# Performance work log

Hardware: AMD Instinct MI355X
Metric: run time of the kernel (lower is better)

## Reference

```python
import jax, jax.numpy as jnp
import numpy as np

B = 64        # BATCH_SIZE
C_IN = 16
L = 8192
FFT0 = 64
FFT1 = 256
CO = 32       # c_out per fft branch (c_out=64 / 2 ffts)
RATIO = FFT1 // FFT0  # 4
EPS = 1e-5


def setup_inputs() -> dict:
    key = jax.random.key(0)
    ks = jax.random.split(key, 12)
    x = jax.random.normal(ks[0], (B, C_IN, L), jnp.float32)
    bn_gamma = 1.0 + 0.1 * jax.random.normal(ks[1], (2, B), jnp.float32)
    bn_beta = 0.1 * jax.random.normal(ks[2], (2, B), jnp.float32)
    mk_r = 0.1 * jax.random.normal(ks[3], (RATIO, RATIO), jnp.float32)
    mk_i = 0.1 * jax.random.normal(ks[4], (RATIO, RATIO), jnp.float32)
    mb_r = 0.1 * jax.random.normal(ks[5], (RATIO,), jnp.float32)
    mb_i = 0.1 * jax.random.normal(ks[6], (RATIO,), jnp.float32)
    fk0_r = 0.1 * jax.random.normal(ks[7], (FFT0 // 2 + 1, C_IN, CO), jnp.float32)
    fk0_i = 0.1 * jax.random.normal(ks[8], (FFT0 // 2 + 1, C_IN, CO), jnp.float32)
    fk1_r = 0.1 * jax.random.normal(ks[9], (FFT1 // 2 + 1, C_IN, CO), jnp.float32)
    fk1_i = 0.1 * jax.random.normal(ks[10], (FFT1 // 2 + 1, C_IN, CO), jnp.float32)
    pbias = 0.1 * jax.random.normal(ks[11], (2 * CO,), jnp.float32)
    return dict(x=x, bn_gamma=bn_gamma, bn_beta=bn_beta, mk_r=mk_r, mk_i=mk_i,
                mb_r=mb_r, mb_i=mb_i, fk0_r=fk0_r, fk0_i=fk0_i,
                fk1_r=fk1_r, fk1_i=fk1_i, pbias=pbias)


def _stft(x2d, n):
    # torch.stft(center=True, pad_mode='reflect', hop=n_fft, rect window),
    # then keep onesided bins and drop the last frame (as in the module).
    N = x2d.shape[0]
    xp = jnp.pad(x2d, ((0, 0), (n // 2, n // 2)), mode='reflect')
    frames = xp.reshape(N, -1, n)               # (N, T+1, n), hop == n_fft
    spec = jnp.fft.rfft(frames, axis=-1)        # onesided == [:, :, :n//2+1]
    return spec[:, :-1, :]                      # drop last frame -> (N, T, n//2+1)


def _zero_interp(p, ratio, out_f):
    # interleave (ratio-1) zeros along the freq axis, then crop to out_f bins
    b, t, f, c = p.shape
    z = jnp.zeros((b, t, f, ratio - 1, c), p.dtype)
    q = jnp.concatenate([p[:, :, :, None, :], z], axis=3).reshape(b, t, f * ratio, c)
    return q[:, :, :out_f, :]


def _cbn(xc, g, b):
    # BatchNorm2d(BATCH_SIZE) after permute(3,0,1,2): channel dim == batch dim,
    # stats over (c_in, T, F) per batch element; complex mean, |.|^2 variance.
    mu = jnp.mean(xc, axis=(1, 2, 3), keepdims=True)
    d = xc - mu
    var = jnp.mean((d * jnp.conj(d)).real, axis=(1, 2, 3), keepdims=True)
    xh = d / jnp.sqrt(var + EPS)
    return xh * g[:, None, None, None] + b[:, None, None, None]


def _istft(out, n):
    # out: (B, T, F, CO) complex. Mirrors permute/reshape + frame repeat + istft
    # (hop=n_fft, rect window, center=True -> trim n//2 on both ends).
    Bq, T, F, Co = out.shape
    pf = out.transpose(0, 3, 2, 1).reshape(Bq * Co, F, T)
    pf = jnp.concatenate([pf, pf[:, :, :1]], axis=-1)   # append copy of frame 0 -> T+1 frames
    fr = jnp.fft.irfft(pf, n=n, axis=1)                 # (N, n, T+1)
    sig = fr.transpose(0, 2, 1).reshape(Bq * Co, -1)    # overlap-add trivial (hop=n)
    sig = sig[:, n // 2: n // 2 + T * n]                # length L
    return sig.reshape(Bq, Co, -1).transpose(0, 2, 1)   # (B, L, CO)


def _forward(x, bn_gamma, bn_beta, mk_r, mk_i, mb_r, mb_i,
             fk0_r, fk0_i, fk1_r, fk1_i, pbias):
    x2 = x.reshape(B * C_IN, L)

    def spec(n):
        s = _stft(x2, n)                                 # (B*C_IN, T, n//2+1)
        T = s.shape[1]
        return s.reshape(B, C_IN, T, n // 2 + 1).transpose(0, 2, 3, 1)  # (B,T,F,C_IN)

    p0 = spec(FFT0)   # (B, 128, 33, 16)
    p1 = spec(FFT1)   # (B, 32, 129, 16)

    # attention merge across time (small fft -> large fft scale)
    pm = p0.reshape(B, -1, RATIO, FFT0 // 2 + 1, C_IN).transpose(0, 1, 3, 4, 2)  # (B,T1,F0,C,r)
    kc = mk_r + 1j * mk_i
    att = jnp.einsum('btfcr,rs->btfcs', pm, kc) + (mb_r + 1j * mb_i)
    a = jax.nn.softmax(jnp.abs(att), axis=-1)            # real weights (complex(a,0) in torch)
    merged = jnp.sum(pm * a, axis=-1) * float(RATIO)     # (B, T1, F0, C_IN)

    F1 = FFT1 // 2 + 1
    mask01 = _zero_interp(jnp.ones(merged.shape, jnp.float32), RATIO, F1)
    up = _zero_interp(merged, RATIO, F1)

    acc0 = p0                                            # own-scale mask is all ones
    acc1 = mask01 * up + (1.0 - mask01) * p1             # cross-scale + complementary mask

    def head(acc, g, b, fkr, fki, n):
        xbn = _cbn(acc, g, b)
        out = jnp.einsum('btfi,fio->btfo', xbn, fkr + 1j * fki)  # FILTER_FLAG merge
        return _istft(out, n)

    t0 = head(acc0, bn_gamma[0], bn_beta[0], fk0_r, fk0_i, FFT0)  # (B, L, CO)
    t1 = head(acc1, bn_gamma[1], bn_beta[1], fk1_r, fk1_i, FFT1)  # (B, L, CO)

    y = jnp.concatenate([t0, t1], axis=2) + pbias        # + patch_bias.real
    y = jax.nn.relu(y)                                   # ACT_DOMAIN == 'time'
    return y.transpose(0, 2, 1)                          # (B, c_out, L)


def reference(x, bn_gamma, bn_beta, mk_r, mk_i, mb_r, mb_i,
              fk0_r, fk0_i, fk1_r, fk1_i, pbias):
    return _forward(x, bn_gamma, bn_beta, mk_r, mk_i, mb_r, mb_i,
                    fk0_r, fk0_i, fk1_r, fk1_i, pbias)
```

## Files before the change

### kernel.cpp

```cpp
#include <hip/hip_runtime.h>
#include <math.h>

#define BB   64
#define CIN  16
#define LL   8192
#define CO   32
#define TCO  64
constexpr int T0n = 128;
constexpr int T1n = 32;
constexpr int F0n = 33;
constexpr int F1n = 129;

typedef unsigned int   uint32;
typedef unsigned short u16;
typedef __attribute__((ext_vector_type(8))) _Float16 half8;
typedef __attribute__((ext_vector_type(4))) float    f32x4;
typedef __attribute__((ext_vector_type(4))) uint32   u32x4;

__device__ inline int imin(int a, int b) { return a < b ? a : b; }

__device__ inline half8 flip_pm(half8 v) {
    u32x4 u;
    __builtin_memcpy(&u, &v, 16);
    u.y ^= 0x80008000u;
    u.w ^= 0x80008000u;
    half8 r;
    __builtin_memcpy(&r, &u, 16);
    return r;
}

template<int N, int F, int TFR, int NTILES, int KTT, int MT_W, int NT_W,
         int NT_STRIDE, bool MT_SPLIT>
__global__ __launch_bounds__(256)
void stft_mfma_kernel(const float* __restrict__ x,
                      const u16* __restrict__ dhi, const u16* __restrict__ dlo,
                      float* __restrict__ p) {
    constexpr int PADN = N + 8;
    __shared__ __align__(16) u16 Xhi[TFR * PADN];
    __shared__ __align__(16) u16 Xlo[TFR * PADN];
    int bc = blockIdx.x;
    const float* xrow = x + (size_t)bc * LL;

    for (int i = threadIdx.x; i < TFR * N; i += 256) {
        int row = i / N, colk = i % N;
        int gi = i - N / 2;
        gi = gi < 0 ? -gi : gi;
        float v = xrow[gi];
        _Float16 h = (_Float16)v;
        _Float16 l = (_Float16)(v - (float)h);
        Xhi[row * PADN + colk] = *(u16*)&h;
        Xlo[row * PADN + colk] = *(u16*)&l;
    }
    __syncthreads();

    int lane = threadIdx.x & 63, w = threadIdx.x >> 6;
    int col = lane & 15, quad = lane >> 4;
    f32x4 acc[MT_W][NT_W];
    #pragma unroll
    for (int mi = 0; mi < MT_W; ++mi)
        #pragma unroll
        for (int nj = 0; nj < NT_W; ++nj) {
            f32x4 z = {0.f, 0.f, 0.f, 0.f};
            acc[mi][nj] = z;
        }

    for (int kt = 0; kt < KTT; ++kt) {
        half8 ah[MT_W], al[MT_W];
        #pragma unroll
        for (int mi = 0; mi < MT_W; ++mi) {
            int mt = MT_SPLIT ? (w * MT_W + mi) : mi;
            int t  = mt * 16 + col;
            ah[mi] = *(const half8*)&Xhi[t * PADN + kt * 32 + quad * 8];
            al[mi] = *(const half8*)&Xlo[t * PADN + kt * 32 + quad * 8];
        }
        #pragma unroll
        for (int nj = 0; nj < NT_W; ++nj) {
            int nt = MT_SPLIT ? nj : (w + nj * NT_STRIDE);
            if (nt < NTILES) {
                half8 bh = ((const half8*)dhi)[(nt * KTT + kt) * 64 + lane];
                half8 bl = ((const half8*)dlo)[(nt * KTT + kt) * 64 + lane];
                #pragma unroll
                for (int mi = 0; mi < MT_W; ++mi) {
                    acc[mi][nj] = __builtin_amdgcn_mfma_f32_16x16x32_f16(ah[mi], bh, acc[mi][nj], 0, 0, 0);
                    acc[mi][nj] = __builtin_amdgcn_mfma_f32_16x16x32_f16(ah[mi], bl, acc[mi][nj], 0, 0, 0);
                    acc[mi][nj] = __builtin_amdgcn_mfma_f32_16x16x32_f16(al[mi], bh, acc[mi][nj], 0, 0, 0);
                }
            }
        }
    }

    int b = bc / CIN, c = bc % CIN;
    #pragma unroll
    for (int mi = 0; mi < MT_W; ++mi) {
        int mt = MT_SPLIT ? (w * MT_W + mi) : mi;
        #pragma unroll
        for (int nj = 0; nj < NT_W; ++nj) {
            int nt = MT_SPLIT ? nj : (w + nj * NT_STRIDE);
            if (nt < NTILES) {
                int j = nt * 16 + col;
                if (j < 2 * F) {
                    int t0 = mt * 16 + quad * 4;
                    f32x4 a = acc[mi][nj];
                    #pragma unroll
                    for (int r = 0; r < 4; ++r) {
                        p[(((size_t)b * TFR + t0 + r) * CIN + c) * (2 * F) + j] = a[r];
                    }
                }
            }
        }
    }
}

__global__ __launch_bounds__(256)
void init_d_kernel(u16* __restrict__ dhi0, u16* __restrict__ dlo0,
                   u16* __restrict__ dhi1, u16* __restrict__ dlo1) {
    int idx = blockIdx.x * 256 + threadIdx.x;
    constexpr int SZ0 = 5 * 2 * 64 * 8;
    constexpr int SZ1 = 17 * 8 * 64 * 8;
    int N, F, KTT, id; u16 *dh, *dl;
    if (idx < SZ0)            { N = 64;  F = F0n; KTT = 2; dh = dhi0; dl = dlo0; id = idx; }
    else if (idx < SZ0 + SZ1) { N = 256; F = F1n; KTT = 8; dh = dhi1; dl = dlo1; id = idx - SZ0; }
    else return;
    int jj   = id & 7;
    int lane = (id >> 3) & 63;
    int rest = id >> 9;
    int kt   = rest % KTT;
    int nt   = rest / KTT;
    int j = nt * 16 + (lane & 15);
    int k = kt * 32 + (lane >> 4) * 8 + jj;
    float v = 0.f;
    if (j < 2 * F) {
        int f = j >> 1;
        int u = (f * k) % N;
        double th = 6.283185307179586476925286766559 * (double)u / (double)N;
        v = (float)((j & 1) ? -sin(th) : cos(th));
    }
    _Float16 h = (_Float16)v;
    _Float16 l = (_Float16)(v - (float)h);
    dh[id] = *(u16*)&h;
    dl[id] = *(u16*)&l;
}

__global__ __launch_bounds__(256)
void merge_kernel(const float2* __restrict__ p0, float2* __restrict__ p1,
                  const float* __restrict__ mkr, const float* __restrict__ mki,
                  const float* __restrict__ mbr, const float* __restrict__ mbi) {
    int idx = blockIdx.x * 256 + threadIdx.x;
    const int total = BB * T1n * CIN * F0n;
    if (idx >= total) return;
    int f0 = idx % F0n; int r1 = idx / F0n;
    int c  = r1 % CIN;  int r2 = r1 / CIN;
    int t1 = r2 % T1n;  int b  = r2 / T1n;
    float2 pm[4];
    #pragma unroll
    for (int r = 0; r < 4; ++r) {
        int t = t1 * 4 + r;
        pm[r] = p0[(((size_t)b * T0n + t) * CIN + c) * F0n + f0];
    }
    float mag[4], mx = -1e30f;
    #pragma unroll
    for (int s = 0; s < 4; ++s) {
        float atr = mbr[s], ati = mbi[s];
        #pragma unroll
        for (int r = 0; r < 4; ++r) {
            float kr = mkr[r * 4 + s], ki = mki[r * 4 + s];
            atr = fmaf(pm[r].x, kr, atr); atr = fmaf(-pm[r].y, ki, atr);
            ati = fmaf(pm[r].x, ki, ati); ati = fmaf(pm[r].y, kr, ati);
        }
        mag[s] = sqrtf(atr * atr + ati * ati);
        mx = fmaxf(mx, mag[s]);
    }
    float se = 0.f;
    #pragma unroll
    for (int s = 0; s < 4; ++s) { mag[s] = expf(mag[s] - mx); se += mag[s]; }
    float inv = 4.0f / se;
    float mr = 0.f, mi = 0.f;
    #pragma unroll
    for (int r = 0; r < 4; ++r) { mr = fmaf(pm[r].x, mag[r], mr); mi = fmaf(pm[r].y, mag[r], mi); }
    p1[(((size_t)b * T1n + t1) * CIN + c) * F1n + 4 * f0] = make_float2(mr * inv, mi * inv);
}

__global__ __launch_bounds__(256)
void cbn_partial_kernel(const float2* __restrict__ p0, const float2* __restrict__ p1,
                        float4* __restrict__ part) {
    int blk  = blockIdx.x;
    int c8   = blk & 7;
    int b    = (blk >> 3) & 63;
    int head = blk >> 9;
    int Nel  = head ? (T1n * CIN * F1n) : (T0n * CIN * F0n);
    const float2* base = head ? (p1 + (size_t)b * (T1n * CIN * F1n))
                              : (p0 + (size_t)b * (T0n * CIN * F0n));
    int chunk = (Nel + 7) / 8;
    int i0 = c8 * chunk, i1 = imin(i0 + chunk, Nel);
    float sr = 0.f, si = 0.f, s2 = 0.f;
    for (int i = i0 + threadIdx.x; i < i1; i += 256) {
        float2 v = base[i];
        sr += v.x; si += v.y;
        s2 = fmaf(v.x, v.x, s2); s2 = fmaf(v.y, v.y, s2);
    }
    __shared__ float red[3][256];
    red[0][threadIdx.x] = sr; red[1][threadIdx.x] = si; red[2][threadIdx.x] = s2;
    __syncthreads();
    for (int off = 128; off > 0; off >>= 1) {
        if (threadIdx.x < off) {
            red[0][threadIdx.x] += red[0][threadIdx.x + off];
            red[1][threadIdx.x] += red[1][threadIdx.x + off];
            red[2][threadIdx.x] += red[2][threadIdx.x + off];
        }
        __syncthreads();
    }
    if (threadIdx.x == 0)
        part[blk] = make_float4(red[0][0], red[1][0], red[2][0], 0.f);
}

__global__ __launch_bounds__(128)
void cbn_final_kernel(const float4* __restrict__ part,
                      const float* __restrict__ gamma, const float* __restrict__ beta,
                      float4* __restrict__ bn) {
    int hb = threadIdx.x;
    float sr = 0.f, si = 0.f, s2 = 0.f;
    #pragma unroll
    for (int c = 0; c < 8; ++c) {
        float4 v = part[hb * 8 + c];
        sr += v.x; si += v.y; s2 += v.z;
    }
    int head = hb >> 6;
    int Nel  = head ? (T1n * CIN * F1n) : (T0n * CIN * F0n);
    float invN = 1.f / (float)Nel;
    float mur = sr * invN, mui = si * invN;
    float var = s2 * invN - mur * mur - mui * mui;
    float g = gamma[hb] * rsqrtf(var + 1e-5f);
    bn[hb] = make_float4(g, beta[hb] - mur * g, -mui * g, 0.f);
}

__global__ __launch_bounds__(256)
void init_w_kernel(u16* __restrict__ whi0, u16* __restrict__ wlo0,
                   u16* __restrict__ whi1, u16* __restrict__ wlo1) {
    int idx = blockIdx.x * 256 + threadIdx.x;
    constexpr int SZ0 = 2 * 3 * 64 * 8;
    constexpr int SZ1 = 8 * 9 * 64 * 8;
    int N, F, KT, id; u16 *dh, *dl;
    if (idx < SZ0)            { N = 64;  F = F0n; KT = 3; dh = whi0; dl = wlo0; id = idx; }
    else if (idx < SZ0 + SZ1) { N = 256; F = F1n; KT = 9; dh = whi1; dl = wlo1; id = idx - SZ0; }
    else return;
    int j    = id & 7;
    int lane = (id >> 3) & 63;
    int rest = id >> 9;
    int kt   = rest % KT;
    int mt   = rest / KT;
    int m  = mt * 16 + (lane & 15);
    int k2 = kt * 32 + (lane >> 4) * 8 + j;
    float v = 0.f;
    if (k2 < 2 * F) {
        int f = k2 >> 1;
        double scale = (f == 0 || f == F - 1) ? (1024.0 / N) : (2048.0 / N);
        int u = (m * f) % N;
        double th = 6.283185307179586476925286766559 * (double)u / (double)N;
        v = (float)((k2 & 1) ? (-scale * sin(th)) : (scale * cos(th)));
    }
    _Float16 h = (_Float16)v;
    _Float16 l = (_Float16)(v - (float)h);
    dh[id] = *(u16*)&h;
    dl[id] = *(u16*)&l;
}

__global__ __launch_bounds__(256)
void init_fk_kernel(const float* __restrict__ r0, const float* __restrict__ i0,
                    const float* __restrict__ r1, const float* __restrict__ i1,
                    float4* __restrict__ q0, float4* __restrict__ q1,
                    float2* __restrict__ s0, float2* __restrict__ s1) {
    int idx = blockIdx.x * 256 + threadIdx.x;
    constexpr int NQ0 = 8 * F0n * 32;
    constexpr int NQ1 = 8 * F1n * 32;
    constexpr int NS0 = F0n * 32;
    constexpr int NS1 = F1n * 32;
    if (idx < NQ0) {
        int id = idx;
        int c2 = id / (F0n * 32); int rem = id % (F0n * 32);
        int o = rem / F0n, f = rem % F0n;
        int s = (f * CIN + 2 * c2) * CO + o;
        q0[id] = make_float4(r0[s], i0[s], r0[s + CO], i0[s + CO]);
    } else if (idx < NQ0 + NQ1) {
        int id = idx - NQ0;
        int c2 = id / (F1n * 32); int rem = id % (F1n * 32);
        int o = rem / F1n, f = rem % F1n;
        int s = (f * CIN + 2 * c2) * CO + o;
        q1[id] = make_float4(r1[s], i1[s], r1[s + CO], i1[s + CO]);
    } else if (idx < NQ0 + NQ1 + NS0) {
        int id = idx - NQ0 - NQ1;
        int o = id / F0n, f = id % F0n;
        float sr = 0.f, si = 0.f;
        for (int ci = 0; ci < CIN; ++ci) {
            int s = (f * CIN + ci) * CO + o;
            sr += r0[s]; si += i0[s];
        }
        s0[id] = make_float2(sr, si);
    } else if (idx < NQ0 + NQ1 + NS0 + NS1) {
        int id = idx - NQ0 - NQ1 - NS0;
        int o = id / F1n, f = id % F1n;
        float sr = 0.f, si = 0.f;
        for (int ci = 0; ci < CIN; ++ci) {
            int s = (f * CIN + ci) * CO + o;
            sr += r1[s]; si += i1[s];
        }
        s1[id] = make_float2(sr, si);
    }
}

template<int F, int TFR, int CH0, int G, int PADW>
__global__ __launch_bounds__(256)
void einsum_kernel(const float2* __restrict__ p, const float4* __restrict__ fkq,
                   const float2* __restrict__ fks, const float4* __restrict__ bn,
                   uint32* __restrict__ Ghi, uint32* __restrict__ Glo) {
    constexpr int FCO = F * 32;
    constexpr int NG  = TFR / G;
    __shared__ float2 xs[G][CIN * F];
    int grp = blockIdx.x % NG, b = blockIdx.x / NG;
    float4 par = bn[(CH0 ? 1 : 0) * BB + b];
    {
        const float4* a4 = (const float4*)(p + ((size_t)b * TFR + (size_t)grp * G) * CIN * F);
        float4* x4 = (float4*)&xs[0][0];
        for (int i = threadIdx.x; i < G * CIN * F / 2; i += 256) x4[i] = a4[i];
    }
    __syncthreads();
    size_t bt0 = (size_t)b * TFR + (size_t)grp * G;
    for (int i = threadIdx.x; i < FCO; i += 256) {
        int o = i / F, f = i - o * F;
        float4 kk[8];
        #pragma unroll
        for (int c2 = 0; c2 < 8; ++c2) kk[c2] = fkq[c2 * FCO + i];
        float2 fv = fks[i];
        float base_re = fmaf(par.y, fv.x, -par.z * fv.y);
        float base_im = fmaf(par.y, fv.y,  par.z * fv.x);
        #pragma unroll
        for (int g = 0; g < G; ++g) {
            float re = 0.f, im = 0.f;
            #pragma unroll
            for (int c2 = 0; c2 < 8; ++c2) {
                float2 xa = xs[g][(2 * c2) * F + f];
                float2 xb = xs[g][(2 * c2 + 1) * F + f];
                float4 kkc = kk[c2];
                re = fmaf(xa.x, kkc.x, re); re = fmaf(-xa.y, kkc.y, re);
                im = fmaf(xa.x, kkc.y, im); im = fmaf(xa.y, kkc.x, im);
                re = fmaf(xb.x, kkc.z, re); re = fmaf(-xb.y, kkc.w, re);
                im = fmaf(xb.x, kkc.w, im); im = fmaf(xb.y, kkc.z, im);
            }
            float res = fmaf(par.x, re, base_re) * 32.f;
            float ims = fmaf(par.x, im, base_im) * 32.f;
            _Float16 rh = (_Float16)res; _Float16 rl = (_Float16)(res - (float)rh);
            _Float16 ih = (_Float16)ims; _Float16 il = (_Float16)(ims - (float)ih);
            size_t d = ((bt0 + g) * 32 + o) * PADW + f;
            Ghi[d] = ((uint32)(*(u16*)&ih) << 16) | (uint32)(*(u16*)&rh);
            Glo[d] = ((uint32)(*(u16*)&il) << 16) | (uint32)(*(u16*)&rl);
        }
    }
    constexpr int PADC = PADW - F;
    for (int j = threadIdx.x; j < G * 32 * PADC; j += 256) {
        int g = j / (32 * PADC); int r = j - g * (32 * PADC);
        int o = r / PADC;        int c = r - o * PADC;
        size_t d = ((bt0 + g) * 32 + o) * PADW + F + c;
        Ghi[d] = 0; Glo[d] = 0;
    }
}

template<int N, int F, int TFR, int CH0, int KT, int FRC, int WMT, bool NTSPLIT>
__global__ __launch_bounds__(256)
void irfft_kernel(const uint32* __restrict__ Ghi, const uint32* __restrict__ Glo,
                  const u16* __restrict__ whi, const u16* __restrict__ wlo,
                  const float* __restrict__ pbias, float* __restrict__ out) {
    constexpr int PADW = KT * 16;
    constexpr int LDW  = PADW + 4;
    constexpr int RW4  = PADW / 4;
    constexpr int NLD  = (32 * RW4 + 255) / 256;
    constexpr int NCH  = (TFR + 1 + FRC - 1) / FRC;
    constexpr int WNT  = NTSPLIT ? 1 : 2;
    __shared__ __align__(16) uint32 buf[2][32 * LDW];

    int ch = blockIdx.x % NCH, b = blockIdx.x / NCH;
    int ft0 = ch * FRC, ftend = imin(ft0 + FRC, TFR + 1);
    int lane = threadIdx.x & 63, w = threadIdx.x >> 6;
    int col = lane & 15, quad = lane >> 4;

    float4 rh[NLD], rl[NLD];
    auto stage_load = [&](int ft) {
        int tf = (ft == TFR) ? 0 : ft;
        const float4* sH = (const float4*)(Ghi + ((size_t)b * TFR + tf) * 32 * PADW);
        const float4* sL = (const float4*)(Glo + ((size_t)b * TFR + tf) * 32 * PADW);
        #pragma unroll
        for (int q = 0; q < NLD; ++q) {
            int i = threadIdx.x + q * 256;
            if (i < 32 * RW4) { rh[q] = sH[i]; rl[q] = sL[i]; }
        }
    };
    auto stage_write = [&]() {
        #pragma unroll
        for (int q = 0; q < NLD; ++q) {
            int i = threadIdx.x + q * 256;
            if (i < 32 * RW4) {
                int row = i / RW4, c = i - row * RW4;
                *(float4*)&buf[0][row * LDW + 4 * c] = rh[q];
                *(float4*)&buf[1][row * LDW + 4 * c] = rl[q];
            }
        }
    };

    stage_load(ft0);
    stage_write();
    __syncthreads();

    const u16* bufh = (const u16*)&buf[0][0];
    const u16* bufl = (const u16*)&buf[1][0];
    constexpr float UNSCALE = 1.0f / 32768.0f;
    size_t bb = (size_t)b * TCO;

    for (int ft = ft0; ft < ftend; ++ft) {
        bool nxt = (ft + 1 < ftend);
        if (nxt) stage_load(ft + 1);

        f32x4 accB[WMT][WNT], accD[WMT][WNT];
        #pragma unroll
        for (int mi = 0; mi < WMT; ++mi)
            #pragma unroll
            for (int nj = 0; nj < WNT; ++nj) {
                f32x4 z = {0.f, 0.f, 0.f, 0.f};
                accB[mi][nj] = z; accD[mi][nj] = z;
            }
        for (int kt = 0; kt < KT; ++kt) {
            half8 bh[WNT], bl[WNT], bhm[WNT], blm[WNT];
            #pragma unroll
            for (int nj = 0; nj < WNT; ++nj) {
                int nt = NTSPLIT ? (w & 1) : nj;
                int ro = (nt * 16 + col) * (2 * LDW) + kt * 32 + quad * 8;
                bh[nj]  = *(const half8*)(bufh + ro);
                bl[nj]  = *(const half8*)(bufl + ro);
                bhm[nj] = flip_pm(bh[nj]);
                blm[nj] = flip_pm(bl[nj]);
            }
            #pragma unroll
            for (int mi = 0; mi < WMT; ++mi) {
                int mt = NTSPLIT ? (w >> 1) : (w * WMT + mi);
                half8 ah = ((const half8*)whi)[(mt * KT + kt) * 64 + lane];
                half8 al = ((const half8*)wlo)[(mt * KT + kt) * 64 + lane];
                #pragma unroll
                for (int nj = 0; nj < WNT; ++nj) {
                    accB[mi][nj] = __builtin_amdgcn_mfma_f32_16x16x32_f16(ah, bh[nj],  accB[mi][nj], 0, 0, 0);
                    accB[mi][nj] = __builtin_amdgcn_mfma_f32_16x16x32_f16(ah, bl[nj],  accB[mi][nj], 0, 0, 0);
                    accB[mi][nj] = __builtin_amdgcn_mfma_f32_16x16x32_f16(al, bh[nj],  accB[mi][nj], 0, 0, 0);
                    accD[mi][nj] = __builtin_amdgcn_mfma_f32_16x16x32_f16(ah, bhm[nj], accD[mi][nj], 0, 0, 0);
                    accD[mi][nj] = __builtin_amdgcn_mfma_f32_16x16x32_f16(ah, blm[nj], accD[mi][nj], 0, 0, 0);
                    accD[mi][nj] = __builtin_amdgcn_mfma_f32_16x16x32_f16(al, bhm[nj], accD[mi][nj], 0, 0, 0);
                }
            }
        }
        #pragma unroll
        for (int mi = 0; mi < WMT; ++mi) {
            int mt = NTSPLIT ? (w >> 1) : (w * WMT + mi);
            #pragma unroll
            for (int hh = 0; hh < 2; ++hh) {
                int m  = mt * 16 + quad * 4 + hh * (N / 2);
                int l0 = ft * N + m - N / 2;
                if ((unsigned)l0 < LL) {
                    #pragma unroll
                    for (int nj = 0; nj < WNT; ++nj) {
                        int nt = NTSPLIT ? (w & 1) : nj;
                        int chn = CH0 + nt * 16 + col;
                        float pb = pbias[chn];
                        f32x4 a = hh ? accD[mi][nj] : accB[mi][nj];
                        float4 v;
                        v.x = fmaxf(fmaf(a[0], UNSCALE, pb), 0.f);
                        v.y = fmaxf(fmaf(a[1], UNSCALE, pb), 0.f);
                        v.z = fmaxf(fmaf(a[2], UNSCALE, pb), 0.f);
                        v.w = fmaxf(fmaf(a[3], UNSCALE, pb), 0.f);
                        *(float4*)(out + (bb + chn) * LL + l0) = v;
                    }
                }
            }
        }
        __syncthreads();
        if (nxt) stage_write();
        __syncthreads();
    }
}

extern "C" void kernel_launch(void* const* d_in, const int* in_sizes, int n_in,
                              void* d_out, int out_size, void* d_ws, size_t ws_size,
                              hipStream_t stream) {
    const float* x     = (const float*)d_in[0];
    const float* gam   = (const float*)d_in[1];
    const float* bet   = (const float*)d_in[2];
    const float* mkr   = (const float*)d_in[3];
    const float* mki   = (const float*)d_in[4];
    const float* mbr   = (const float*)d_in[5];
    const float* mbi   = (const float*)d_in[6];
    const float* fk0r  = (const float*)d_in[7];
    const float* fk0i  = (const float*)d_in[8];
    const float* fk1r  = (const float*)d_in[9];
    const float* fk1i  = (const float*)d_in[10];
    const float* pbias = (const float*)d_in[11];
    float* out = (float*)d_out;

    float2* p0   = (float2*)d_ws;
    float2* p1   = p0 + (size_t)BB * T0n * CIN * F0n;
    float4* bnp  = (float4*)(p1 + (size_t)BB * T1n * CIN * F1n);
    float4* part = bnp + 2 * BB;
    float4* fkq0 = part + 1024;
    float4* fkq1 = fkq0 + 8 * F0n * 32;
    float2* fks0 = (float2*)(fkq1 + 8 * F1n * 32);
    float2* fks1 = fks0 + F0n * 32;
    uint32* Ghi  = (uint32*)(fks1 + F1n * 32);
    uint32* Glo  = Ghi + (size_t)8192 * 32 * 48;
    u16*    whi0 = (u16*)(Glo + (size_t)8192 * 32 * 48);
    u16*    wlo0 = whi0 + 3072;
    u16*    whi1 = wlo0 + 3072;
    u16*    wlo1 = whi1 + 36864;
    u16*    dhi0 = wlo1 + 36864;
    u16*    dlo0 = dhi0 + 5120;
    u16*    dhi1 = dlo0 + 5120;
    u16*    dlo1 = dhi1 + 69632;

    init_w_kernel<<<(3072 + 36864 + 255) / 256, 256, 0, stream>>>(whi0, wlo0, whi1, wlo1);
    init_d_kernel<<<(5120 + 69632 + 255) / 256, 256, 0, stream>>>(dhi0, dlo0, dhi1, dlo1);
    init_fk_kernel<<<(8 * (F0n + F1n) * 32 + (F0n + F1n) * 32 + 255) / 256, 256, 0, stream>>>(
        fk0r, fk0i, fk1r, fk1i, fkq0, fkq1, fks0, fks1);
    stft_mfma_kernel<64, F0n, 128, 5, 2, 2, 5, 1, true><<<BB * CIN, 256, 0, stream>>>(
        x, dhi0, dlo0, (float*)p0);
    stft_mfma_kernel<256, F1n, 32, 17, 8, 2, 5, 4, false><<<BB * CIN, 256, 0, stream>>>(
        x, dhi1, dlo1, (float*)p1);
    merge_kernel<<<(BB * T1n * CIN * F0n) / 256, 256, 0, stream>>>(p0, p1, mkr, mki, mbr, mbi);
    cbn_partial_kernel<<<1024, 256, 0, stream>>>(p0, p1, part);
    cbn_final_kernel<<<1, 128, 0, stream>>>(part, gam, bet, bnp);
    einsum_kernel<F1n, T1n, 32, 4, 144><<<BB * (T1n / 4), 256, 0, stream>>>(
        p1, fkq1, fks1, bnp, Ghi, Glo);
    irfft_kernel<256, F1n, T1n, 32, 9, 9, 2, false><<<BB * 4, 256, 0, stream>>>(
        Ghi, Glo, whi1, wlo1, pbias, out);
    einsum_kernel<F0n, T0n, 0, 8, 48><<<BB * (T0n / 8), 256, 0, stream>>>(
        p0, fkq0, fks0, bnp, Ghi, Glo);
    irfft_kernel<64, F0n, T0n, 0, 3, 17, 1, true><<<BB * 8, 256, 0, stream>>>(
        Ghi, Glo, whi0, wlo0, pbias, out);
}
```

Baseline: 517.6 us.

## Retile einsum over frequency chunks and run irfft one frame per block

```diff
diff --git a/kernel.cpp b/kernel.cpp
--- a/kernel.cpp
+++ b/kernel.cpp
@@ -307,178 +307,158 @@
     }
 }
 
-template<int F, int TFR, int CH0, int G, int PADW>
+template<int F, int TFR, int CH0, int FCH, int BTB>
 __global__ __launch_bounds__(256)
 void einsum_kernel(const float2* __restrict__ p, const float4* __restrict__ fkq,
                    const float2* __restrict__ fks, const float4* __restrict__ bn,
                    uint32* __restrict__ Ghi, uint32* __restrict__ Glo) {
-    constexpr int FCO = F * 32;
-    constexpr int NG  = TFR / G;
-    __shared__ float2 xs[G][CIN * F];
-    int grp = blockIdx.x % NG, b = blockIdx.x / NG;
+    constexpr int FCO  = F * 32;
+    constexpr int NFCH = (F + FCH - 1) / FCH;
+    static_assert(FCH == 8 && BTB * CIN * FCH % 256 == 0, "cfg");
+    __shared__ float2 xs[BTB][CIN][FCH];
+    int fch = blockIdx.x % NFCH;
+    int b   = blockIdx.x / NFCH;
+    int f0  = fch * FCH;
+    int o   = threadIdx.x >> 3;
+    int fl  = threadIdx.x & 7;
+    int f   = f0 + fl;
+    bool valid = f < F;
+    int fc = valid ? f : F - 1;
+    float4 kk[8];
+    #pragma unroll
+    for (int c2 = 0; c2 < 8; ++c2) kk[c2] = fkq[c2 * FCO + o * F + fc];
+    float2 fv = fks[o * F + fc];
     float4 par = bn[(CH0 ? 1 : 0) * BB + b];
-    {
-        const float4* a4 = (const float4*)(p + ((size_t)b * TFR + (size_t)grp * G) * CIN * F);
-        float4* x4 = (float4*)&xs[0][0];
-        for (int i = threadIdx.x; i < G * CIN * F / 2; i += 256) x4[i] = a4[i];
-    }
-    __syncthreads();
-    size_t bt0 = (size_t)b * TFR + (size_t)grp * G;
-    for (int i = threadIdx.x; i < FCO; i += 256) {
-        int o = i / F, f = i - o * F;
-        float4 kk[8];
-        #pragma unroll
-        for (int c2 = 0; c2 < 8; ++c2) kk[c2] = fkq[c2 * FCO + i];
-        float2 fv = fks[i];
-        float base_re = fmaf(par.y, fv.x, -par.z * fv.y);
-        float base_im = fmaf(par.y, fv.y,  par.z * fv.x);
-        #pragma unroll
-        for (int g = 0; g < G; ++g) {
+    float base_re = fmaf(par.y, fv.x, -par.z * fv.y);
+    float base_im = fmaf(par.y, fv.y,  par.z * fv.x);
+
+    for (int t0 = 0; t0 < TFR; t0 += BTB) {
+        const float2* pb = p + (size_t)(b * TFR + t0) * CIN * F;
+        for (int i = threadIdx.x; i < BTB * CIN * FCH; i += 256) {
+            int fi = i & 7;
+            int r  = i >> 3;
+            int ff = f0 + fi;
+            ((float2*)xs)[i] = (ff < F) ? pb[(size_t)r * F + ff] : make_float2(0.f, 0.f);
+        }
+        __syncthreads();
+        for (int tp = 0; tp < BTB; ++tp) {
             float re = 0.f, im = 0.f;
             #pragma unroll
             for (int c2 = 0; c2 < 8; ++c2) {
-                float2 xa = xs[g][(2 * c2) * F + f];
-                float2 xb = xs[g][(2 * c2 + 1) * F + f];
+                float2 xa = xs[tp][2 * c2][fl];
+                float2 xb = xs[tp][2 * c2 + 1][fl];
                 float4 kkc = kk[c2];
                 re = fmaf(xa.x, kkc.x, re); re = fmaf(-xa.y, kkc.y, re);
                 im = fmaf(xa.x, kkc.y, im); im = fmaf(xa.y, kkc.x, im);
                 re = fmaf(xb.x, kkc.z, re); re = fmaf(-xb.y, kkc.w, re);
                 im = fmaf(xb.x, kkc.w, im); im = fmaf(xb.y, kkc.z, im);
             }
-            float res = fmaf(par.x, re, base_re) * 32.f;
-            float ims = fmaf(par.x, im, base_im) * 32.f;
-            _Float16 rh = (_Float16)res; _Float16 rl = (_Float16)(res - (float)rh);
-            _Float16 ih = (_Float16)ims; _Float16 il = (_Float16)(ims - (float)ih);
-            size_t d = ((bt0 + g) * 32 + o) * PADW + f;
-            Ghi[d] = ((uint32)(*(u16*)&ih) << 16) | (uint32)(*(u16*)&rh);
-            Glo[d] = ((uint32)(*(u16*)&il) << 16) | (uint32)(*(u16*)&rl);
-        }
-    }
-    constexpr int PADC = PADW - F;
-    for (int j = threadIdx.x; j < G * 32 * PADC; j += 256) {
-        int g = j / (32 * PADC); int r = j - g * (32 * PADC);
-        int o = r / PADC;        int c = r - o * PADC;
-        size_t d = ((bt0 + g) * 32 + o) * PADW + F + c;
-        Ghi[d] = 0; Glo[d] = 0;
-    }
-}
-
-template<int N, int F, int TFR, int CH0, int KT, int FRC, int WMT, bool NTSPLIT>
+            if (valid) {
+                float res = fmaf(par.x, re, base_re) * 32.f;
+                float ims = fmaf(par.x, im, base_im) * 32.f;
+                _Float16 rh = (_Float16)res; _Float16 rl = (_Float16)(res - (float)rh);
+                _Float16 ih = (_Float16)ims; _Float16 il = (_Float16)(ims - (float)ih);
+                size_t d = ((size_t)(b * TFR + t0 + tp) * 32 + o) * F + f;
+                Ghi[d] = ((uint32)(*(u16*)&ih) << 16) | (uint32)(*(u16*)&rh);
+                Glo[d] = ((uint32)(*(u16*)&il) << 16) | (uint32)(*(u16*)&rl);
+            }
+        }
+        __syncthreads();
+    }
+}
+
+template<int N, int F, int TFR, int CH0, int KT, int WMT, bool NTSPLIT>
 __global__ __launch_bounds__(256)
 void irfft_kernel(const uint32* __restrict__ Ghi, const uint32* __restrict__ Glo,
                   const u16* __restrict__ whi, const u16* __restrict__ wlo,
                   const float* __restrict__ pbias, float* __restrict__ out) {
     constexpr int PADW = KT * 16;
     constexpr int LDW  = PADW + 4;
-    constexpr int RW4  = PADW / 4;
-    constexpr int NLD  = (32 * RW4 + 255) / 256;
-    constexpr int NCH  = (TFR + 1 + FRC - 1) / FRC;
     constexpr int WNT  = NTSPLIT ? 1 : 2;
     __shared__ __align__(16) uint32 buf[2][32 * LDW];
-
-    int ch = blockIdx.x % NCH, b = blockIdx.x / NCH;
-    int ft0 = ch * FRC, ftend = imin(ft0 + FRC, TFR + 1);
+    int t  = blockIdx.x % (TFR + 1);
+    int b  = blockIdx.x / (TFR + 1);
+    int tf = (t == TFR) ? 0 : t;
+    const uint32* sH = Ghi + (size_t)(b * TFR + tf) * 32 * F;
+    const uint32* sL = Glo + (size_t)(b * TFR + tf) * 32 * F;
+    for (int i = threadIdx.x; i < 32 * F; i += 256) {
+        int row = i / F, c = i - row * F;
+        buf[0][row * LDW + c] = sH[i];
+        buf[1][row * LDW + c] = sL[i];
+    }
+    for (int i = threadIdx.x; i < 32 * (PADW - F); i += 256) {
+        constexpr int cols = PADW - F;
+        int row = i / cols, c = i - row * cols;
+        buf[0][row * LDW + F + c] = 0;
+        buf[1][row * LDW + F + c] = 0;
+    }
+    __syncthreads();
+
     int lane = threadIdx.x & 63, w = threadIdx.x >> 6;
     int col = lane & 15, quad = lane >> 4;
-
-    float4 rh[NLD], rl[NLD];
-    auto stage_load = [&](int ft) {
-        int tf = (ft == TFR) ? 0 : ft;
-        const float4* sH = (const float4*)(Ghi + ((size_t)b * TFR + tf) * 32 * PADW);
-        const float4* sL = (const float4*)(Glo + ((size_t)b * TFR + tf) * 32 * PADW);
-        #pragma unroll
-        for (int q = 0; q < NLD; ++q) {
-            int i = threadIdx.x + q * 256;
-            if (i < 32 * RW4) { rh[q] = sH[i]; rl[q] = sL[i]; }
-        }
-    };
-    auto stage_write = [&]() {
-        #pragma unroll
-        for (int q = 0; q < NLD; ++q) {
-            int i = threadIdx.x + q * 256;
-            if (i < 32 * RW4) {
-                int row = i / RW4, c = i - row * RW4;
-                *(float4*)&buf[0][row * LDW + 4 * c] = rh[q];
-                *(float4*)&buf[1][row * LDW + 4 * c] = rl[q];
-            }
-        }
-    };
-
-    stage_load(ft0);
-    stage_write();
-    __syncthreads();
-
     const u16* bufh = (const u16*)&buf[0][0];
     const u16* bufl = (const u16*)&buf[1][0];
+
+    f32x4 accB[WMT][WNT], accD[WMT][WNT];
+    #pragma unroll
+    for (int mi = 0; mi < WMT; ++mi)
+        #pragma unroll
+        for (int nj = 0; nj < WNT; ++nj) {
+            f32x4 z = {0.f, 0.f, 0.f, 0.f};
+            accB[mi][nj] = z; accD[mi][nj] = z;
+        }
+    for (int kt = 0; kt < KT; ++kt) {
+        half8 bh[WNT], bl[WNT], bhm[WNT], blm[WNT];
+        #pragma unroll
+        for (int nj = 0; nj < WNT; ++nj) {
+            int nt = NTSPLIT ? (w & 1) : nj;
+            int ro = (nt * 16 + col) * (2 * LDW) + kt * 32 + quad * 8;
+            bh[nj]  = *(const half8*)(bufh + ro);
+            bl[nj]  = *(const half8*)(bufl + ro);
+            bhm[nj] = flip_pm(bh[nj]);
+            blm[nj] = flip_pm(bl[nj]);
+        }
+        #pragma unroll
+        for (int mi = 0; mi < WMT; ++mi) {
+            int mt = NTSPLIT ? (w >> 1) : (w * WMT + mi);
+            half8 ah = ((const half8*)whi)[(mt * KT + kt) * 64 + lane];
+            half8 al = ((const half8*)wlo)[(mt * KT + kt) * 64 + lane];
+            #pragma unroll
+            for (int nj = 0; nj < WNT; ++nj) {
+                accB[mi][nj] = __builtin_amdgcn_mfma_f32_16x16x32_f16(ah, bh[nj],  accB[mi][nj], 0, 0, 0);
+                accB[mi][nj] = __builtin_amdgcn_mfma_f32_16x16x32_f16(ah, bl[nj],  accB[mi][nj], 0, 0, 0);
+                accB[mi][nj] = __builtin_amdgcn_mfma_f32_16x16x32_f16(al, bh[nj],  accB[mi][nj], 0, 0, 0);
+                accD[mi][nj] = __builtin_amdgcn_mfma_f32_16x16x32_f16(ah, bhm[nj], accD[mi][nj], 0, 0, 0);
+                accD[mi][nj] = __builtin_amdgcn_mfma_f32_16x16x32_f16(ah, blm[nj], accD[mi][nj], 0, 0, 0);
+                accD[mi][nj] = __builtin_amdgcn_mfma_f32_16x16x32_f16(al, bhm[nj], accD[mi][nj], 0, 0, 0);
+            }
+        }
+    }
     constexpr float UNSCALE = 1.0f / 32768.0f;
     size_t bb = (size_t)b * TCO;
-
-    for (int ft = ft0; ft < ftend; ++ft) {
-        bool nxt = (ft + 1 < ftend);
-        if (nxt) stage_load(ft + 1);
-
-        f32x4 accB[WMT][WNT], accD[WMT][WNT];
-        #pragma unroll
-        for (int mi = 0; mi < WMT; ++mi)
-            #pragma unroll
-            for (int nj = 0; nj < WNT; ++nj) {
-                f32x4 z = {0.f, 0.f, 0.f, 0.f};
-                accB[mi][nj] = z; accD[mi][nj] = z;
-            }
-        for (int kt = 0; kt < KT; ++kt) {
-            half8 bh[WNT], bl[WNT], bhm[WNT], blm[WNT];
-            #pragma unroll
-            for (int nj = 0; nj < WNT; ++nj) {
-                int nt = NTSPLIT ? (w & 1) : nj;
-                int ro = (nt * 16 + col) * (2 * LDW) + kt * 32 + quad * 8;
-                bh[nj]  = *(const half8*)(bufh + ro);
-                bl[nj]  = *(const half8*)(bufl + ro);
-                bhm[nj] = flip_pm(bh[nj]);
-                blm[nj] = flip_pm(bl[nj]);
-            }
-            #pragma unroll
-            for (int mi = 0; mi < WMT; ++mi) {
-                int mt = NTSPLIT ? (w >> 1) : (w * WMT + mi);
-                half8 ah = ((const half8*)whi)[(mt * KT + kt) * 64 + lane];
-                half8 al = ((const half8*)wlo)[(mt * KT + kt) * 64 + lane];
+    #pragma unroll
+    for (int mi = 0; mi < WMT; ++mi) {
+        int mt = NTSPLIT ? (w >> 1) : (w * WMT + mi);
+        #pragma unroll
+        for (int hh = 0; hh < 2; ++hh) {
+            int m  = mt * 16 + quad * 4 + hh * (N / 2);
+            int l0 = t * N + m - N / 2;
+            if ((unsigned)l0 < LL) {
                 #pragma unroll
                 for (int nj = 0; nj < WNT; ++nj) {
-                    accB[mi][nj] = __builtin_amdgcn_mfma_f32_16x16x32_f16(ah, bh[nj],  accB[mi][nj], 0, 0, 0);
-                    accB[mi][nj] = __builtin_amdgcn_mfma_f32_16x16x32_f16(ah, bl[nj],  accB[mi][nj], 0, 0, 0);
-                    accB[mi][nj] = __builtin_amdgcn_mfma_f32_16x16x32_f16(al, bh[nj],  accB[mi][nj], 0, 0, 0);
-                    accD[mi][nj] = __builtin_amdgcn_mfma_f32_16x16x32_f16(ah, bhm[nj], accD[mi][nj], 0, 0, 0);
-                    accD[mi][nj] = __builtin_amdgcn_mfma_f32_16x16x32_f16(ah, blm[nj], accD[mi][nj], 0, 0, 0);
-                    accD[mi][nj] = __builtin_amdgcn_mfma_f32_16x16x32_f16(al, bhm[nj], accD[mi][nj], 0, 0, 0);
+                    int nt = NTSPLIT ? (w & 1) : nj;
+                    int chn = CH0 + nt * 16 + col;
+                    float pb = pbias[chn];
+                    f32x4 a = hh ? accD[mi][nj] : accB[mi][nj];
+                    float4 v;
+                    v.x = fmaxf(fmaf(a[0], UNSCALE, pb), 0.f);
+                    v.y = fmaxf(fmaf(a[1], UNSCALE, pb), 0.f);
+                    v.z = fmaxf(fmaf(a[2], UNSCALE, pb), 0.f);
+                    v.w = fmaxf(fmaf(a[3], UNSCALE, pb), 0.f);
+                    *(float4*)(out + (bb + chn) * LL + l0) = v;
                 }
             }
         }
-        #pragma unroll
-        for (int mi = 0; mi < WMT; ++mi) {
-            int mt = NTSPLIT ? (w >> 1) : (w * WMT + mi);
-            #pragma unroll
-            for (int hh = 0; hh < 2; ++hh) {
-                int m  = mt * 16 + quad * 4 + hh * (N / 2);
-                int l0 = ft * N + m - N / 2;
-                if ((unsigned)l0 < LL) {
-                    #pragma unroll
-                    for (int nj = 0; nj < WNT; ++nj) {
-                        int nt = NTSPLIT ? (w & 1) : nj;
-                        int chn = CH0 + nt * 16 + col;
-                        float pb = pbias[chn];
-                        f32x4 a = hh ? accD[mi][nj] : accB[mi][nj];
-                        float4 v;
-                        v.x = fmaxf(fmaf(a[0], UNSCALE, pb), 0.f);
-                        v.y = fmaxf(fmaf(a[1], UNSCALE, pb), 0.f);
-                        v.z = fmaxf(fmaf(a[2], UNSCALE, pb), 0.f);
-                        v.w = fmaxf(fmaf(a[3], UNSCALE, pb), 0.f);
-                        *(float4*)(out + (bb + chn) * LL + l0) = v;
-                    }
-                }
-            }
-        }
-        __syncthreads();
-        if (nxt) stage_write();
-        __syncthreads();
     }
 }
 
@@ -508,8 +488,8 @@
     float2* fks0 = (float2*)(fkq1 + 8 * F1n * 32);
     float2* fks1 = fks0 + F0n * 32;
     uint32* Ghi  = (uint32*)(fks1 + F1n * 32);
-    uint32* Glo  = Ghi + (size_t)8192 * 32 * 48;
-    u16*    whi0 = (u16*)(Glo + (size_t)8192 * 32 * 48);
+    uint32* Glo  = Ghi + (size_t)BB * T0n * 32 * F0n;
+    u16*    whi0 = (u16*)(Glo + (size_t)BB * T0n * 32 * F0n);
     u16*    wlo0 = whi0 + 3072;
     u16*    whi1 = wlo0 + 3072;
     u16*    wlo1 = whi1 + 36864;
@@ -529,12 +509,12 @@
     merge_kernel<<<(BB * T1n * CIN * F0n) / 256, 256, 0, stream>>>(p0, p1, mkr, mki, mbr, mbi);
     cbn_partial_kernel<<<1024, 256, 0, stream>>>(p0, p1, part);
     cbn_final_kernel<<<1, 128, 0, stream>>>(part, gam, bet, bnp);
-    einsum_kernel<F1n, T1n, 32, 4, 144><<<BB * (T1n / 4), 256, 0, stream>>>(
+    einsum_kernel<F1n, T1n, 32, 8, 16><<<17 * BB, 256, 0, stream>>>(
         p1, fkq1, fks1, bnp, Ghi, Glo);
-    irfft_kernel<256, F1n, T1n, 32, 9, 9, 2, false><<<BB * 4, 256, 0, stream>>>(
+    irfft_kernel<256, F1n, T1n, 32, 9, 2, false><<<BB * (T1n + 1), 256, 0, stream>>>(
         Ghi, Glo, whi1, wlo1, pbias, out);
-    einsum_kernel<F0n, T0n, 0, 8, 48><<<BB * (T0n / 8), 256, 0, stream>>>(
+    einsum_kernel<F0n, T0n, 0, 8, 16><<<5 * BB, 256, 0, stream>>>(
         p0, fkq0, fks0, bnp, Ghi, Glo);
-    irfft_kernel<64, F0n, T0n, 0, 3, 17, 1, true><<<BB * 8, 256, 0, stream>>>(
+    irfft_kernel<64, F0n, T0n, 0, 3, 1, true><<<BB * (T0n + 1), 256, 0, stream>>>(
         Ghi, Glo, whi0, wlo0, pbias, out);
 }
```

New measurement: 503.6 us. -2.7%, faster.
